# Kernel optimization log

Hardware: AMD Instinct MI355X
Metric: run time of the kernel (lower is better)

The kernel has to match this reference:

```python
import jax, jax.numpy as jnp
import numpy as np
from jax import lax

S = 2                      # window half-size (matches init_kwargs s)
K = 2 * S + 1              # kernel size = 5
SZ = float(K ** 3)         # number of voxels in the window
EPS = 1e-10


def _box_sum(x):
    """Replicate-pad then valid 3D box-sum with an all-ones K^3 kernel.
    x: [N, 1, D, H, W] -> [N, 1, D, H, W]. Same math as F.pad(mode='replicate')
    followed by Conv3d(ones kernel, valid)."""
    xp = jnp.pad(x, ((0, 0), (0, 0), (S, S), (S, S), (S, S)), mode='edge')
    kern = jnp.ones((1, 1, K, K, K), dtype=x.dtype)
    return lax.conv_general_dilated(
        xp, kern, window_strides=(1, 1, 1), padding='VALID',
        dimension_numbers=('NCDHW', 'OIDHW', 'NCDHW'))


def setup_inputs() -> dict:
    key = jax.random.key(0)
    k1, k2 = jax.random.split(key)
    shape = (2, 1, 160, 160, 160)
    im_fixed = jax.random.normal(k1, shape, dtype=jnp.float32)
    im_moving = jax.random.normal(k2, shape, dtype=jnp.float32)
    mask = jnp.ones(shape, dtype=jnp.float32)
    return {"im_fixed": im_fixed, "im_moving": im_moving, "mask": mask}


def reference(im_fixed, im_moving, mask):
    # local means
    u_F = _box_sum(im_fixed) / SZ
    u_M = _box_sum(im_moving) / SZ
    # local variances (box-sum of squared centered values, then / SZ)
    sigma_F = jnp.sqrt(_box_sum((im_fixed - u_F) ** 2) / SZ)
    sigma_M = jnp.sqrt(_box_sum((im_moving - u_M) ** 2) / SZ)
    # normalized images
    n_F = (im_fixed - u_F) / (sigma_F + EPS)
    n_M = (im_moving - u_M) / (sigma_M + EPS)
    # local cross-correlation map (box-sum, NOT divided by SZ, as in torch code)
    cross = _box_sum(n_F * n_M)
    # reduce: negative masked sum of squared LCC
    return -1.0 * jnp.sum(cross ** 2 * mask)
```

## Files before the change

kernel.cpp:

```cpp
#include <hip/hip_runtime.h>

namespace {

constexpr int LEN   = 160;
constexpr int PLANE = LEN * LEN;
constexpr int VOL   = LEN * PLANE;
constexpr float INV_SZ = 1.0f / 125.0f;
constexpr float EPS_   = 1e-10f;

constexpr int BLK = 512;

constexpr int FTX = 32, FTY = 16, FZC = 32;
constexpr int FRX = FTX + 4, FRY = FTY + 4;
constexpr int FNRAW = FRX * FRY;
constexpr int FNBX = 5, FNBY = 10, FNXY = 50, FNCHZ = 5;

constexpr int STX = 32, STY = 32, SZC = 16;
constexpr int SRX = STX + 4, SRY = STY + 4;
constexpr int SNRAW = SRX * SRY;
constexpr int SNBX = 5, SNBY = 5, SNXY = 25, SNCHZ = 10;

constexpr int QW = 62, RW = 4;

__device__ __forceinline__ int clampi(int v) {
  return v < 0 ? 0 : (v > LEN - 1 ? LEN - 1 : v);
}

__device__ __forceinline__ int swz(int g) {
  const int xcd = g & 7, idx = g >> 3;
  return (xcd < RW) ? xcd * (QW + 1) + idx
                    : RW * (QW + 1) + (xcd - RW) * QW + idx;
}

__global__ __launch_bounds__(BLK) void fuseAB(const float* __restrict__ inA,
                                              const float* __restrict__ inB,
                                              float* __restrict__ outP) {
  __shared__ __align__(16) float raw[2][2][2][FRY][FRX];
  __shared__ __align__(16) float xs [2][4][2][FRY][FTX];
  constexpr int RAWB = 2 * 2 * FRY * FRX;
  constexpr int XSB  = 4 * 2 * FRY * FTX;
  constexpr int AS   = 2 * FRY * FTX;
  constexpr int PS   = FRY * FTX;

  const int tid = threadIdx.x;
  const int g = blockIdx.x + FNBX * (blockIdx.y + FNBY * blockIdx.z);
  const int w = swz(g);
  const int batch = w / 250, rem = w % 250;
  const int zc = rem / FNXY, tl = rem % FNXY;
  const int x0 = (tl % FNBX) * FTX;
  const int y0 = (tl / FNBX) * FTY;
  const int z0 = zc * FZC;
  const size_t base = (size_t)batch * VOL;

  int off[2]; float* ld0[2][2][2];
  bool act[2];
#pragma unroll
  for (int j = 0; j < 2; ++j) {
    int i = tid + j * BLK;
    act[j] = i < FNRAW;
    int ii = act[j] ? i : 0;
    const int ry = ii / FRX, rx = ii % FRX;
    off[j] = clampi(y0 - 2 + ry) * LEN + clampi(x0 - 2 + rx);
#pragma unroll
    for (int f = 0; f < 2; ++f)
#pragma unroll
      for (int p = 0; p < 2; ++p) ld0[j][f][p] = &raw[0][f][p][ry][rx];
  }

  const float* ts0[2]; float* td0[2];
#pragma unroll
  for (int k = 0; k < 2; ++k) {
    int tt = (k == 0) ? tid : tid + BLK;
    if (tt >= 640) tt = 0;
    const int p = tt / 320, r1 = tt % 320;
    const int f = r1 / 160, r2 = r1 % 160;
    const int r = r2 / 8,  c = r2 % 8;
    ts0[k] = &raw[0][f][p][r][4 * c];
    td0[k] = &xs[0][f][p][r][4 * c];
  }

  const bool qact = tid < 256;
  const int ly  = tid >> 4;
  const int lx0 = (tid & 15) * 2;
  const int sOff = (y0 + ly) * LEN + (x0 + lx0);
  const float* yb0 = &xs[0][0][0][ly][lx0];

  float s0A[2][2], s0B[2][2], s1A[2][2], s1B[2][2];
  float2 rzF[6], rzM[6], rzF2[6], rzM2[6];
  float2 cnF[4], cnM[4];

  auto loadPair = [&](int t, float (&ra)[2][2], float (&rb)[2][2]) {
#pragma unroll
    for (int p = 0; p < 2; ++p) {
      const size_t pb = base + (size_t)clampi(t + p) * PLANE;
#pragma unroll
      for (int j = 0; j < 2; ++j)
        if (act[j]) { ra[p][j] = inA[pb + off[j]]; rb[p][j] = inB[pb + off[j]]; }
    }
  };
  auto depositPair = [&](int buf, float (&ra)[2][2], float (&rb)[2][2]) {
#pragma unroll
    for (int p = 0; p < 2; ++p)
#pragma unroll
      for (int j = 0; j < 2; ++j)
        if (act[j]) {
          ld0[j][0][p][buf * RAWB] = ra[p][j];
          ld0[j][1][p][buf * RAWB] = rb[p][j];
        }
  };

  auto xsumTask = [&](int buf, int k) {
    const float* src = ts0[k] + buf * RAWB;
    float* dst = td0[k] + buf * XSB;
    const float4 u = *(const float4*)src;
    const float4 v = *(const float4*)(src + 4);
    const float m = u.y + u.z + u.w;
    float4 s;
    s.x = m + u.x + v.x;
    s.y = m + v.x + v.y;
    s.z = s.y - u.y + v.z;
    s.w = s.z - u.z + v.w;
    *(float4*)dst = s;
    float4 uq, vq;
    uq.x = u.x * u.x; uq.y = u.y * u.y; uq.z = u.z * u.z; uq.w = u.w * u.w;
    vq.x = v.x * v.x; vq.y = v.y * v.y; vq.z = v.z * v.z; vq.w = v.w * v.w;
    const float mq = uq.y + uq.z + uq.w;
    float4 q;
    q.x = mq + uq.x + vq.x;
    q.y = mq + vq.x + vq.y;
    q.z = q.y - uq.y + vq.z;
    q.w = q.z - uq.z + vq.w;
    *(float4*)(dst + 2 * AS) = q;
  };

  auto body = [&](int buf, int t,
                  float (&dA)[2][2], float (&dB)[2][2],
                  float (&lA)[2][2], float (&lB)[2][2]) {
    if (t + 2 <= z0 + FZC) depositPair(buf ^ 1, dA, dB);
    if (t + 4 <= z0 + FZC) loadPair(t + 4, lA, lB);

    xsumTask(buf, 0);
    if (tid < 128) xsumTask(buf, 1);

    if (qact) {
      cnF[0] = cnF[2]; cnF[1] = cnF[3]; cnM[0] = cnM[2]; cnM[1] = cnM[3];
      cnF[2] = *(const float2*)&raw[buf][0][0][ly + 2][lx0 + 2];
      cnF[3] = *(const float2*)&raw[buf][0][1][ly + 2][lx0 + 2];
      cnM[2] = *(const float2*)&raw[buf][1][0][ly + 2][lx0 + 2];
      cnM[3] = *(const float2*)&raw[buf][1][1][ly + 2][lx0 + 2];
    }

    __syncthreads();

    if (qact) {
#pragma unroll
      for (int s = 0; s < 4; ++s) {
        rzF[s] = rzF[s + 2]; rzM[s] = rzM[s + 2];
        rzF2[s] = rzF2[s + 2]; rzM2[s] = rzM2[s + 2];
      }
      const float* yb = yb0 + buf * XSB;
#pragma unroll
      for (int p = 0; p < 2; ++p) {
        float2 sf = {0.f, 0.f}, sm = {0.f, 0.f};
        float2 sf2 = {0.f, 0.f}, sm2 = {0.f, 0.f};
#pragma unroll
        for (int k = 0; k < 5; ++k) {
          const float2 a  = *(const float2*)(yb + 0 * AS + p * PS + k * FTX);
          const float2 b  = *(const float2*)(yb + 1 * AS + p * PS + k * FTX);
          const float2 a2 = *(const float2*)(yb + 2 * AS + p * PS + k * FTX);
          const float2 b2 = *(const float2*)(yb + 3 * AS + p * PS + k * FTX);
          sf.x += a.x;   sf.y += a.y;   sm.x += b.x;   sm.y += b.y;
          sf2.x += a2.x; sf2.y += a2.y; sm2.x += b2.x; sm2.y += b2.y;
        }
        rzF[4 + p] = sf; rzM[4 + p] = sm;
        rzF2[4 + p] = sf2; rzM2[4 + p] = sm2;
      }

      if (t >= z0 + 2) {
#pragma unroll
        for (int q = 0; q < 2; ++q) {
          const int zo = t - 2 + q;
          float2 bF = {0.f, 0.f}, bM = {0.f, 0.f};
          float2 bF2 = {0.f, 0.f}, bM2 = {0.f, 0.f};
#pragma unroll
          for (int s = 0; s < 5; ++s) {
            bF.x += rzF[q + s].x;   bF.y += rzF[q + s].y;
            bM.x += rzM[q + s].x;   bM.y += rzM[q + s].y;
            bF2.x += rzF2[q + s].x; bF2.y += rzF2[q + s].y;
            bM2.x += rzM2[q + s].x; bM2.y += rzM2[q + s].y;
          }
          float2 o;
          {
            const float uF = bF.x * INV_SZ, uM = bM.x * INV_SZ;
            const float vF = fmaxf(bF2.x * INV_SZ - uF * uF, 0.f);
            const float vM = fmaxf(bM2.x * INV_SZ - uM * uM, 0.f);
            o.x = ((cnF[q].x - uF) * (cnM[q].x - uM)) /
                  ((sqrtf(vF) + EPS_) * (sqrtf(vM) + EPS_));
          }
          {
            const float uF = bF.y * INV_SZ, uM = bM.y * INV_SZ;
            const float vF = fmaxf(bF2.y * INV_SZ - uF * uF, 0.f);
            const float vM = fmaxf(bM2.y * INV_SZ - uM * uM, 0.f);
            o.y = ((cnF[q].y - uF) * (cnM[q].y - uM)) /
                  ((sqrtf(vF) + EPS_) * (sqrtf(vM) + EPS_));
          }
          *(float2*)&outP[base + (size_t)zo * PLANE + sOff] = o;
        }
      }
    }
  };

  loadPair(z0 - 2, s0A, s0B);
  depositPair(0, s0A, s0B);
  loadPair(z0, s1A, s1B);
  __syncthreads();

  for (int t = z0 - 2; t <= z0 + FZC; t += 4) {
    body(0, t,     s1A, s1B, s0A, s0B);
    body(1, t + 2, s0A, s0B, s1A, s1B);
  }
}

__global__ __launch_bounds__(BLK) void slab1_reduce(const float* __restrict__ p,
                                                    const float* __restrict__ mask,
                                                    float* __restrict__ out) {
  __shared__ __align__(16) float raw[2][2][SRY][SRX];
  __shared__ __align__(16) float xs [2][2][SRY][SRX];
  __shared__ float wsum[BLK / 64];
  constexpr int RAWB = 2 * SRY * SRX;

  const int tid = threadIdx.x;
  const int g = blockIdx.x + SNBX * (blockIdx.y + SNBY * blockIdx.z);
  const int w = swz(g);
  const int batch = w / 250, rem = w % 250;
  const int zc = rem / SNXY, tl = rem % SNXY;
  const int x0 = (tl % SNBX) * STX;
  const int y0 = (tl / SNBX) * STY;
  const int z0 = zc * SZC;
  const size_t base = (size_t)batch * VOL;

  int off[3]; float* ld0[3][2];
  bool act[3];
#pragma unroll
  for (int j = 0; j < 3; ++j) {
    int i = tid + j * BLK;
    act[j] = i < SNRAW;
    int ii = act[j] ? i : 0;
    const int ry = ii / SRX, rx = ii % SRX;
    off[j] = clampi(y0 - 2 + ry) * LEN + clampi(x0 - 2 + rx);
#pragma unroll
    for (int pp = 0; pp < 2; ++pp) ld0[j][pp] = &raw[0][pp][ry][rx];
  }
  const int ly  = tid >> 4;
  const int lx0 = (tid & 15) * 2;

  float s0[2][3], s1[2][3];
  float2 rz[6];
  float acc = 0.f;

  auto loadPair = [&](int t, float (&r)[2][3]) {
#pragma unroll
    for (int pp = 0; pp < 2; ++pp) {
      const size_t pb = base + (size_t)clampi(t + pp) * PLANE;
#pragma unroll
      for (int j = 0; j < 3; ++j)
        if (act[j]) r[pp][j] = p[pb + off[j]];
    }
  };
  auto depositPair = [&](int buf, float (&r)[2][3]) {
#pragma unroll
    for (int pp = 0; pp < 2; ++pp)
#pragma unroll
      for (int j = 0; j < 3; ++j)
        if (act[j]) ld0[j][pp][buf * RAWB] = r[pp][j];
  };

  auto body = [&](int buf, int t, float (&dep)[2][3], float (&ld)[2][3]) {
    if (t + 2 <= z0 + SZC) depositPair(buf ^ 1, dep);
    if (t + 4 <= z0 + SZC) loadPair(t + 4, ld);

    if (tid < 288) {
      const int c = tid & 7, r = tid >> 3;
#pragma unroll
      for (int pp = 0; pp < 2; ++pp) {
        const float* rp = &raw[buf][pp][r][4 * c];
        const float4 u = *(const float4*)rp;
        const float4 v = *(const float4*)(rp + 4);
        const float m = u.y + u.z + u.w;
        float4 s;
        s.x = m + u.x + v.x;
        s.y = m + v.x + v.y;
        s.z = s.y - u.y + v.z;
        s.w = s.z - u.z + v.w;
        *(float4*)&xs[buf][pp][r][4 * c] = s;
      }
    }

    __syncthreads();

#pragma unroll
    for (int s = 0; s < 4; ++s) rz[s] = rz[s + 2];
#pragma unroll
    for (int pp = 0; pp < 2; ++pp) {
      float2 s2 = {0.f, 0.f};
#pragma unroll
      for (int k = 0; k < 5; ++k) {
        const float2 a = *(const float2*)&xs[buf][pp][ly + k][lx0];
        s2.x += a.x; s2.y += a.y;
      }
      rz[4 + pp] = s2;
    }

    if (t >= z0 + 2) {
#pragma unroll
      for (int q = 0; q < 2; ++q) {
        const int zo = t - 2 + q;
        float2 bs = {0.f, 0.f};
#pragma unroll
        for (int s = 0; s < 5; ++s) { bs.x += rz[q + s].x; bs.y += rz[q + s].y; }
        const size_t gg = base + (size_t)zo * PLANE +
                          (size_t)(y0 + ly) * LEN + (x0 + lx0);
        const float2 mk = *(const float2*)&mask[gg];
        acc += bs.x * bs.x * mk.x + bs.y * bs.y * mk.y;
      }
    }
  };

  loadPair(z0 - 2, s0);
  depositPair(0, s0);
  loadPair(z0, s1);
  __syncthreads();

  for (int t = z0 - 2; t <= z0 + SZC; t += 4) {
    body(0, t,     s1, s0);
    body(1, t + 2, s0, s1);
  }

#pragma unroll
  for (int o = 32; o > 0; o >>= 1) acc += __shfl_down(acc, o, 64);
  const int lane = tid & 63, wid = tid >> 6;
  if (lane == 0) wsum[wid] = acc;
  __syncthreads();
  if (tid == 0) {
    float tt = 0.f;
#pragma unroll
    for (int ww = 0; ww < BLK / 64; ++ww) tt += wsum[ww];
    atomicAdd(out, -tt);
  }
}

}

extern "C" void kernel_launch(void* const* d_in, const int* in_sizes, int n_in,
                              void* d_out, int out_size, void* d_ws, size_t ws_size,
                              hipStream_t stream) {
  const float* F    = (const float*)d_in[0];
  const float* M    = (const float*)d_in[1];
  const float* mask = (const float*)d_in[2];
  float* out = (float*)d_out;

  float* pB = (float*)d_ws;

  hipMemsetAsync(d_out, 0, sizeof(float), stream);

  dim3 gf(FNBX, FNBY, FNCHZ * 2), blk(BLK);
  dim3 gs(SNBX, SNBY, SNCHZ * 2);

  fuseAB<<<gf, blk, 0, stream>>>(F, M, pB);
  slab1_reduce<<<gs, blk, 0, stream>>>(pB, mask, out);
}
```

Baseline: 162.8 us.

## Split fuseAB block into producer and consumer thread groups

Within the fused first-stage kernel, threads 256-511 now handle all global loads, shared-memory deposits and x-direction sums, while threads 0-255 only do the y/z box sums and the normalised-product output. Previously every thread did some loading and x-summing, and half the threads then sat idle during the consumer phase. The aim is warp specialisation, so that global-load latency overlaps with consumer arithmetic across waves. The cost is that each producer thread issues more loads and holds more registers, and the split may leave the two halves unevenly loaded.

```diff
diff --git a/kernel.cpp b/kernel.cpp
--- a/kernel.cpp
+++ b/kernel.cpp
@@ -14,6 +14,11 @@
 constexpr int FRX = FTX + 4, FRY = FTY + 4;
 constexpr int FNRAW = FRX * FRY;
 constexpr int FNBX = 5, FNBY = 10, FNXY = 50, FNCHZ = 5;
+constexpr int PR   = FRY * FRX;
+constexpr int RAWB = 2 * 2 * PR;
+constexpr int PSX  = FRY * FTX;
+constexpr int AS   = 2 * PSX;
+constexpr int XSB  = 4 * 2 * PSX;
 
 constexpr int STX = 32, STY = 32, SZC = 16;
 constexpr int SRX = STX + 4, SRY = STY + 4;
@@ -37,10 +42,6 @@
                                               float* __restrict__ outP) {
   __shared__ __align__(16) float raw[2][2][2][FRY][FRX];
   __shared__ __align__(16) float xs [2][4][2][FRY][FTX];
-  constexpr int RAWB = 2 * 2 * FRY * FRX;
-  constexpr int XSB  = 4 * 2 * FRY * FTX;
-  constexpr int AS   = 2 * FRY * FTX;
-  constexpr int PS   = FRY * FTX;
 
   const int tid = threadIdx.x;
   const int g = blockIdx.x + FNBX * (blockIdx.y + FNBY * blockIdx.z);
@@ -52,66 +53,64 @@
   const int z0 = zc * FZC;
   const size_t base = (size_t)batch * VOL;
 
-  int off[2]; float* ld0[2][2][2];
-  bool act[2];
-#pragma unroll
-  for (int j = 0; j < 2; ++j) {
-    int i = tid + j * BLK;
-    act[j] = i < FNRAW;
-    int ii = act[j] ? i : 0;
+  const bool prod = tid >= 256;
+  const int  pt   = tid & 255;
+
+  int off[3]; bool ract[3]; float* rld[3];
+#pragma unroll
+  for (int k = 0; k < 3; ++k) {
+    const int i = pt + k * 256;
+    ract[k] = i < FNRAW;
+    const int ii = ract[k] ? i : 0;
     const int ry = ii / FRX, rx = ii % FRX;
-    off[j] = clampi(y0 - 2 + ry) * LEN + clampi(x0 - 2 + rx);
-#pragma unroll
-    for (int f = 0; f < 2; ++f)
-#pragma unroll
-      for (int p = 0; p < 2; ++p) ld0[j][f][p] = &raw[0][f][p][ry][rx];
-  }
-
-  const float* ts0[2]; float* td0[2];
-#pragma unroll
-  for (int k = 0; k < 2; ++k) {
-    int tt = (k == 0) ? tid : tid + BLK;
+    off[k] = clampi(y0 - 2 + ry) * LEN + clampi(x0 - 2 + rx);
+    rld[k] = &raw[0][0][0][ry][rx];
+  }
+  const float* txs[3]; float* txd[3]; bool tact2;
+#pragma unroll
+  for (int k = 0; k < 3; ++k) {
+    int tt = pt + k * 256;
     if (tt >= 640) tt = 0;
     const int p = tt / 320, r1 = tt % 320;
     const int f = r1 / 160, r2 = r1 % 160;
     const int r = r2 / 8,  c = r2 % 8;
-    ts0[k] = &raw[0][f][p][r][4 * c];
-    td0[k] = &xs[0][f][p][r][4 * c];
-  }
-
-  const bool qact = tid < 256;
-  const int ly  = tid >> 4;
-  const int lx0 = (tid & 15) * 2;
+    txs[k] = &raw[0][f][p][r][4 * c];
+    txd[k] = &xs[0][f][p][r][4 * c];
+  }
+  tact2 = (pt + 512) < 640;
+
+  const int ly  = pt >> 4;
+  const int lx0 = (pt & 15) * 2;
   const int sOff = (y0 + ly) * LEN + (x0 + lx0);
   const float* yb0 = &xs[0][0][0][ly][lx0];
 
-  float s0A[2][2], s0B[2][2], s1A[2][2], s1B[2][2];
+  float sA0[3][2], sB0[3][2], sA1[3][2], sB1[3][2];
   float2 rzF[6], rzM[6], rzF2[6], rzM2[6];
   float2 cnF[4], cnM[4];
 
-  auto loadPair = [&](int t, float (&ra)[2][2], float (&rb)[2][2]) {
+  auto loadPair = [&](int t, float (&a)[3][2], float (&b)[3][2]) {
 #pragma unroll
     for (int p = 0; p < 2; ++p) {
       const size_t pb = base + (size_t)clampi(t + p) * PLANE;
 #pragma unroll
-      for (int j = 0; j < 2; ++j)
-        if (act[j]) { ra[p][j] = inA[pb + off[j]]; rb[p][j] = inB[pb + off[j]]; }
-    }
-  };
-  auto depositPair = [&](int buf, float (&ra)[2][2], float (&rb)[2][2]) {
-#pragma unroll
-    for (int p = 0; p < 2; ++p)
-#pragma unroll
-      for (int j = 0; j < 2; ++j)
-        if (act[j]) {
-          ld0[j][0][p][buf * RAWB] = ra[p][j];
-          ld0[j][1][p][buf * RAWB] = rb[p][j];
+      for (int k = 0; k < 3; ++k)
+        if (ract[k]) { a[k][p] = inA[pb + off[k]]; b[k][p] = inB[pb + off[k]]; }
+    }
+  };
+  auto depositPair = [&](int buf, float (&a)[3][2], float (&b)[3][2]) {
+#pragma unroll
+    for (int k = 0; k < 3; ++k)
+      if (ract[k]) {
+#pragma unroll
+        for (int p = 0; p < 2; ++p) {
+          rld[k][buf * RAWB + p * PR]          = a[k][p];
+          rld[k][buf * RAWB + 2 * PR + p * PR] = b[k][p];
         }
-  };
-
+      }
+  };
   auto xsumTask = [&](int buf, int k) {
-    const float* src = ts0[k] + buf * RAWB;
-    float* dst = td0[k] + buf * XSB;
+    const float* src = txs[k] + buf * RAWB;
+    float* dst = txd[k] + buf * XSB;
     const float4 u = *(const float4*)src;
     const float4 v = *(const float4*)(src + 4);
     const float m = u.y + u.z + u.w;
@@ -134,15 +133,15 @@
   };
 
   auto body = [&](int buf, int t,
-                  float (&dA)[2][2], float (&dB)[2][2],
-                  float (&lA)[2][2], float (&lB)[2][2]) {
-    if (t + 2 <= z0 + FZC) depositPair(buf ^ 1, dA, dB);
-    if (t + 4 <= z0 + FZC) loadPair(t + 4, lA, lB);
-
-    xsumTask(buf, 0);
-    if (tid < 128) xsumTask(buf, 1);
-
-    if (qact) {
+                  float (&dA)[3][2], float (&dB)[3][2],
+                  float (&lA)[3][2], float (&lB)[3][2]) {
+    if (prod) {
+      if (t + 2 <= z0 + FZC) depositPair(buf ^ 1, dA, dB);
+      if (t + 4 <= z0 + FZC) loadPair(t + 4, lA, lB);
+      xsumTask(buf, 0);
+      xsumTask(buf, 1);
+      if (tact2) xsumTask(buf, 2);
+    } else {
       cnF[0] = cnF[2]; cnF[1] = cnF[3]; cnM[0] = cnM[2]; cnM[1] = cnM[3];
       cnF[2] = *(const float2*)&raw[buf][0][0][ly + 2][lx0 + 2];
       cnF[3] = *(const float2*)&raw[buf][0][1][ly + 2][lx0 + 2];
@@ -152,7 +151,7 @@
 
     __syncthreads();
 
-    if (qact) {
+    if (!prod) {
 #pragma unroll
       for (int s = 0; s < 4; ++s) {
         rzF[s] = rzF[s + 2]; rzM[s] = rzM[s + 2];
@@ -165,10 +164,10 @@
         float2 sf2 = {0.f, 0.f}, sm2 = {0.f, 0.f};
 #pragma unroll
         for (int k = 0; k < 5; ++k) {
-          const float2 a  = *(const float2*)(yb + 0 * AS + p * PS + k * FTX);
-          const float2 b  = *(const float2*)(yb + 1 * AS + p * PS + k * FTX);
-          const float2 a2 = *(const float2*)(yb + 2 * AS + p * PS + k * FTX);
-          const float2 b2 = *(const float2*)(yb + 3 * AS + p * PS + k * FTX);
+          const float2 a  = *(const float2*)(yb + 0 * AS + p * PSX + k * FTX);
+          const float2 b  = *(const float2*)(yb + 1 * AS + p * PSX + k * FTX);
+          const float2 a2 = *(const float2*)(yb + 2 * AS + p * PSX + k * FTX);
+          const float2 b2 = *(const float2*)(yb + 3 * AS + p * PSX + k * FTX);
           sf.x += a.x;   sf.y += a.y;   sm.x += b.x;   sm.y += b.y;
           sf2.x += a2.x; sf2.y += a2.y; sm2.x += b2.x; sm2.y += b2.y;
         }
@@ -210,14 +209,16 @@
     }
   };
 
-  loadPair(z0 - 2, s0A, s0B);
-  depositPair(0, s0A, s0B);
-  loadPair(z0, s1A, s1B);
+  if (prod) {
+    loadPair(z0 - 2, sA0, sB0);
+    depositPair(0, sA0, sB0);
+    loadPair(z0, sA1, sB1);
+  }
   __syncthreads();
 
   for (int t = z0 - 2; t <= z0 + FZC; t += 4) {
-    body(0, t,     s1A, s1B, s0A, s0B);
-    body(1, t + 2, s0A, s0B, s1A, s1B);
+    body(0, t,     sA1, sB1, sA0, sB0);
+    body(1, t + 2, sA0, sB0, sA1, sB1);
   }
 }
 
@@ -227,7 +228,7 @@
   __shared__ __align__(16) float raw[2][2][SRY][SRX];
   __shared__ __align__(16) float xs [2][2][SRY][SRX];
   __shared__ float wsum[BLK / 64];
-  constexpr int RAWB = 2 * SRY * SRX;
+  constexpr int RAWB1 = 2 * SRY * SRX;
 
   const int tid = threadIdx.x;
   const int g = blockIdx.x + SNBX * (blockIdx.y + SNBY * blockIdx.z);
@@ -272,7 +273,7 @@
     for (int pp = 0; pp < 2; ++pp)
 #pragma unroll
       for (int j = 0; j < 3; ++j)
-        if (act[j]) ld0[j][pp][buf * RAWB] = r[pp][j];
+        if (act[j]) ld0[j][pp][buf * RAWB1] = r[pp][j];
   };
 
   auto body = [&](int buf, int t, float (&dep)[2][3], float (&ld)[2][3]) {
```

After: 158.9 us. -2.4%, faster.
